# Kernel tuning notes

Hardware: AMD Instinct MI355X
Metric: run time of the kernel (lower is better)

## Reference

```python
import jax, jax.numpy as jnp
import numpy as np

B, N, D, H, DH = 4, 2048, 512, 8, 64  # batch, seqlen, hidden, heads, dim-per-head
EPS = 1e-5


def _layer_norm(x, g, b):
    m = jnp.mean(x, axis=-1, keepdims=True)
    v = jnp.var(x, axis=-1, keepdims=True)
    return (x - m) * jax.lax.rsqrt(v + EPS) * g + b


def setup_inputs() -> dict:
    key = jax.random.key(0)
    k0, k1, k2 = jax.random.split(key, 3)
    T = B * N
    return {
        "x": jax.random.normal(k0, (T, D), jnp.float32),
        "ln1_g": jnp.ones((D,), jnp.float32),
        "ln1_b": jnp.zeros((D,), jnp.float32),
        "w_uvqk": jax.random.normal(k1, (D, H * 4 * DH), jnp.float32) * 0.02,
        "ln2_g": jnp.ones((H * DH,), jnp.float32),
        "ln2_b": jnp.zeros((H * DH,), jnp.float32),
        "w_proj": jax.random.normal(k2, (H * DH, D), jnp.float32) * 0.02,
        "scaling_seqlen": N,
    }


def reference(x, ln1_g, ln1_b, w_uvqk, ln2_g, ln2_b, w_proj, scaling_seqlen):
    T = x.shape[0]
    # input layernorm -> fused uvqk projection -> SiLU
    normed_x = _layer_norm(x, ln1_g, ln1_b)
    silu_uvqk = jax.nn.silu(normed_x @ w_uvqk)          # [T, H*4*DH]
    silu_uvqk = silu_uvqk.reshape(T, H, 4 * DH)
    user, value, query, key = jnp.split(silu_uvqk, [DH, 2 * DH, 3 * DH], axis=-1)

    # jagged -> [B, N, H, DH] (equal-length sequences, offsets = i*N)
    q = query.reshape(B, N, H, DH)
    k = key.reshape(B, N, H, DH)
    v = value.reshape(B, N, H, DH)

    # HSTU attention: silu-gated (no softmax), causal, scaled by 1/scaling_seqlen
    scores = jnp.einsum('bnhd,bmhd->bhnm', q, k)        # [B, H, N, N]
    p = jax.nn.silu(scores) / jnp.float32(scaling_seqlen)
    causal = jnp.tril(jnp.ones((N, N), bool))
    p = jnp.where(causal, p, 0.0)
    attn = jnp.einsum('bhnm,bmhd->bnhd', p, v).reshape(T, H * DH)

    # output norm, user gate, projection, residual (dropout p=0.0 -> identity)
    normed_attn = _layer_norm(attn, ln2_g, ln2_b)
    user_flat = user.reshape(T, H * DH)
    out = (normed_attn * user_flat) @ w_proj + x
    return out
```

## Files before the change

kernel.cpp:

```cpp
#include <hip/hip_runtime.h>
#include <hip/hip_bf16.h>

typedef __bf16 bf16;
typedef __attribute__((ext_vector_type(8))) __bf16 bf16x8;
typedef __attribute__((ext_vector_type(4))) float f32x4;

#define BB   4
#define NN   2048
#define DD   512
#define HH   8
#define DHH  64
#define TT   (BB*NN)
#define NUU  (HH*4*DHH)

#define AS1 __attribute__((address_space(1)))
#define AS3 __attribute__((address_space(3)))
__device__ __forceinline__ void gload16(const void* g, void* l){
  __builtin_amdgcn_global_load_lds((const AS1 void*)g, (AS3 void*)l, 16, 0, 0);
}

__device__ __forceinline__ float silu_fast(float x){
  return x * __builtin_amdgcn_rcpf(1.0f + __expf(-x));
}

__global__ void k_transpose_cast(const float* __restrict__ in, bf16* __restrict__ out,
                                 int R, int C){
  __shared__ float tile[32][33];
  int tx = threadIdx.x, ty = threadIdx.y;
  int c0 = blockIdx.x*32, r0 = blockIdx.y*32;
  #pragma unroll
  for (int i=0;i<4;i++) tile[ty+i*8][tx] = in[(size_t)(r0+ty+i*8)*C + c0+tx];
  __syncthreads();
  #pragma unroll
  for (int i=0;i<4;i++) out[(size_t)(c0+ty+i*8)*R + r0+tx] = (bf16)tile[tx][ty+i*8];
}

__global__ void k_ln_cast(const float* __restrict__ x, const float* __restrict__ g,
                          const float* __restrict__ bta, bf16* __restrict__ out){
  int lane = threadIdx.x & 63;
  int row  = blockIdx.x*4 + (threadIdx.x>>6);
  const float* xr = x + (size_t)row*512 + lane*8;
  float4 v0 = *(const float4*)xr;
  float4 v1 = *(const float4*)(xr+4);
  float vv[8] = {v0.x,v0.y,v0.z,v0.w,v1.x,v1.y,v1.z,v1.w};
  float s = 0.f, ss = 0.f;
  #pragma unroll
  for (int j=0;j<8;j++){ s += vv[j]; ss += vv[j]*vv[j]; }
  #pragma unroll
  for (int d=32; d; d>>=1){ s += __shfl_xor(s,d); ss += __shfl_xor(ss,d); }
  float m  = s * (1.f/512.f);
  float vr = ss * (1.f/512.f) - m*m;
  float rs = rsqrtf(vr + 1e-5f);
  const float* gp = g + lane*8;
  const float* bp = bta + lane*8;
  bf16x8 o;
  #pragma unroll
  for (int j=0;j<8;j++) o[j] = (bf16)((vv[j]-m)*rs*gp[j] + bp[j]);
  *(bf16x8*)(out + (size_t)row*512 + lane*8) = o;
}

__global__ void k_ln_gate(const float* __restrict__ attn, const float* __restrict__ g,
                          const float* __restrict__ bta, const bf16* __restrict__ uvqk,
                          bf16* __restrict__ out){
  int lane = threadIdx.x & 63;
  int row  = blockIdx.x*4 + (threadIdx.x>>6);
  const float* xr = attn + (size_t)row*512 + lane*8;
  float4 v0 = *(const float4*)xr;
  float4 v1 = *(const float4*)(xr+4);
  float vv[8] = {v0.x,v0.y,v0.z,v0.w,v1.x,v1.y,v1.z,v1.w};
  float s = 0.f, ss = 0.f;
  #pragma unroll
  for (int j=0;j<8;j++){ s += vv[j]; ss += vv[j]*vv[j]; }
  #pragma unroll
  for (int d=32; d; d>>=1){ s += __shfl_xor(s,d); ss += __shfl_xor(ss,d); }
  float m  = s * (1.f/512.f);
  float vr = ss * (1.f/512.f) - m*m;
  float rs = rsqrtf(vr + 1e-5f);
  const float* gp = g + lane*8;
  const float* bp = bta + lane*8;
  const bf16* up = uvqk + (size_t)row*NUU + (lane>>3)*256 + ((lane*8)&63);
  bf16x8 uu = *(const bf16x8*)up;
  bf16x8 o;
  #pragma unroll
  for (int j=0;j<8;j++)
    o[j] = (bf16)(((vv[j]-m)*rs*gp[j] + bp[j]) * (float)uu[j]);
  *(bf16x8*)(out + (size_t)row*512 + lane*8) = o;
}

template<int EPI>
__global__ __launch_bounds__(256) void k_gemm(const bf16* __restrict__ A,
                                              const bf16* __restrict__ BT,
                                              int Nd, const float* __restrict__ resid,
                                              void* __restrict__ Cout,
                                              bf16* __restrict__ vtout){
  __shared__ __align__(16) char smem[32768];
  char* As = smem;
  char* Bs = smem + 16384;
  const int K = 512;
  int t = threadIdx.x, lane = t & 63, wid = t >> 6;
  int wr = wid >> 1, wc = wid & 1;
  int lin = blockIdx.x;
  int wk  = (lin & 7)*((int)gridDim.x >> 3) + (lin >> 3);
  int nx  = Nd >> 7;
  int m0 = (wk / nx) * 128, n0 = (wk % nx) * 128;
  int blk = (lane & 7) ^ (lane >> 3);
  const bf16* gA = A  + (size_t)(m0 + wid*32 + (lane>>3))*K + blk*8;
  const bf16* gB = BT + (size_t)(n0 + wid*32 + (lane>>3))*K + blk*8;
  f32x4 acc[4][4] = {};
  for (int k0 = 0; k0 < K; k0 += 64){
    __syncthreads();
    #pragma unroll
    for (int c = 0; c < 4; ++c){
      gload16(gA + (size_t)c*8*K, As + wid*4096 + c*1024);
      gload16(gB + (size_t)c*8*K, Bs + wid*4096 + c*1024);
    }
    gA += 64; gB += 64;
    __syncthreads();
    #pragma unroll
    for (int kk = 0; kk < 64; kk += 32){
      int c0 = kk + (lane >> 4) * 8;
      bf16x8 a[4], b[4];
      #pragma unroll
      for (int i = 0; i < 4; i++){
        int ra = wr*64 + i*16 + (lane & 15);
        a[i] = *(const bf16x8*)(As + (((ra*64 + c0)*2) ^ ((ra & 7) << 4)));
        int rb = wc*64 + i*16 + (lane & 15);
        b[i] = *(const bf16x8*)(Bs + (((rb*64 + c0)*2) ^ ((rb & 7) << 4)));
      }
      #pragma unroll
      for (int i = 0; i < 4; i++)
        #pragma unroll
        for (int jj = 0; jj < 4; jj++)
          acc[i][jj] = __builtin_amdgcn_mfma_f32_16x16x32_bf16(a[i], b[jj], acc[i][jj], 0, 0, 0);
    }
  }
  bool isv = (EPI == 0) && ((n0 & 255) == 0) && (wc == 1);
  #pragma unroll
  for (int i = 0; i < 4; i++){
    #pragma unroll
    for (int jj = 0; jj < 4; jj++){
      int col = n0 + wc*64 + jj*16 + (lane & 15);
      if (EPI == 0){
        union { unsigned long long u; ushort s[4]; } pw;
        #pragma unroll
        for (int r = 0; r < 4; r++){
          int rowg = m0 + wr*64 + i*16 + (lane >> 4)*4 + r;
          float sv = silu_fast(acc[i][jj][r]);
          ((bf16*)Cout)[(size_t)rowg*Nd + col] = (bf16)sv;
          pw.s[r] = __builtin_bit_cast(ushort, (bf16)sv);
        }
        if (isv){
          int dh    = jj*16 + (lane & 15);
          int rowg0 = m0 + wr*64 + i*16 + (lane >> 4)*4;
          int bb = rowg0 >> 11, nn = rowg0 & (NN-1);
          int hh = n0 >> 8;
          *(unsigned long long*)(vtout + ((size_t)((bb*HH + hh)*64 + dh)*NN + nn)) = pw.u;
        }
      } else {
        #pragma unroll
        for (int r = 0; r < 4; r++){
          int rowg = m0 + wr*64 + i*16 + (lane >> 4)*4 + r;
          ((float*)Cout)[(size_t)rowg*Nd + col] = acc[i][jj][r] + resid[(size_t)rowg*Nd + col];
        }
      }
    }
  }
}

__global__ __launch_bounds__(512) void k_attn(const bf16* __restrict__ uv,
                                              const bf16* __restrict__ vt,
                                              float* __restrict__ attn,
                                              const int* __restrict__ scal){
  __shared__ __align__(16) char smem[49152];
  char* Ps = smem + 32768;
  int t = threadIdx.x, lane = t & 63, w = t >> 6;
  int lin  = blockIdx.x;
  int work = (lin & 7)*160 + (lin >> 3);
  int grp  = work / 40;
  int d    = 39 - (work % 40);
  int b = grp >> 3, h = grp & 7;
  int qt, ch;
  if (d < 4)       { qt = d;              ch = 0; }
  else if (d < 12) { qt = 4  + (d-4)/2;   ch = (d-4)&1; }
  else if (d < 24) { qt = 8  + (d-12)/3;  ch = (d-12)%3; }
  else             { qt = 12 + (d-24)/4;  ch = (d-24)&3; }
  int j0 = ch*8;
  int jmax = 2*qt + 1;
  int j1 = (jmax < j0+7) ? jmax : j0+7;
  int tok0 = b*NN + qt*128;
  float sinv = 1.0f / (float)(scal[0]);

  int blk  = (lane & 7) ^ (lane >> 3);
  int rsub = lane >> 3;
  {
    const bf16* gq = uv + (size_t)(tok0 + w*16 + rsub)*NUU + h*256 + 128 + blk*8;
    gload16(gq,         Ps + w*2048);
    gload16(gq + 8*NUU, Ps + w*2048 + 1024);
  }
  const bf16* gk = uv + (size_t)(b*NN + j0*64 + w*8 + rsub)*NUU + h*256 + 192 + blk*8;
  const bf16* gv = vt + (size_t)((b*HH + h)*64 + w*8 + rsub)*NN + j0*64 + blk*8;
  gload16(gk, smem + w*1024);
  gload16(gv, smem + 8192 + w*1024);
  gk += (size_t)64*NUU; gv += 64;
  asm volatile("s_waitcnt vmcnt(0)" ::: "memory");
  __builtin_amdgcn_s_barrier();
  bf16x8 qfrag[2];
  {
    int rq = w*16 + (lane & 15);
    #pragma unroll
    for (int kx = 0; kx < 2; ++kx){
      int c0 = kx*32 + (lane >> 4) * 8;
      qfrag[kx] = *(const bf16x8*)(Ps + (((rq*64 + c0)*2) ^ ((rq & 7) << 4)));
    }
  }
  __syncthreads();

  f32x4 oacc[4] = {};
  int qmin = qt*128 + w*16;
  int q_l  = w*16 + (lane & 15);
  int qglob = qt*128 + q_l;
  int cur = 0;
  for (int j = j0; j <= j1; ++j){
    if (j < j1){
      gload16(gk, smem + (cur^1)*16384 + w*1024);
      gload16(gv, smem + (cur^1)*16384 + 8192 + w*1024);
      gk += (size_t)64*NUU; gv += 64;
      asm volatile("s_waitcnt vmcnt(2)" ::: "memory");
    } else {
      asm volatile("s_waitcnt vmcnt(0)" ::: "memory");
    }
    __builtin_amdgcn_s_barrier();
    char* Ks = smem + cur*16384;
    char* Vs = smem + cur*16384 + 8192;
    if (j*64 < qmin + 16){
      f32x4 sacc[4] = {};
      #pragma unroll
      for (int kx = 0; kx < 2; ++kx){
        int c0 = kx*32 + (lane >> 4) * 8;
        #pragma unroll
        for (int ki = 0; ki < 4; ++ki){
          int rk = ki*16 + (lane & 15);
          bf16x8 ak = *(const bf16x8*)(Ks + (((rk*64 + c0)*2) ^ ((rk & 7) << 4)));
          sacc[ki] = __builtin_amdgcn_mfma_f32_16x16x32_bf16(ak, qfrag[kx], sacc[ki], 0, 0, 0);
        }
      }
      if (j*64 + 63 <= qmin){
        #pragma unroll
        for (int ki = 0; ki < 4; ++ki){
          int kvb = ki*16 + (lane >> 4)*4;
          union { unsigned long long u; ushort s[4]; } pw;
          #pragma unroll
          for (int r = 0; r < 4; r++){
            float p = silu_fast(sacc[ki][r]);
            pw.s[r] = __builtin_bit_cast(ushort, (bf16)p);
          }
          *(unsigned long long*)(Ps + (((q_l*64 + kvb)*2) ^ ((q_l & 7) << 4))) = pw.u;
        }
      } else {
        #pragma unroll
        for (int ki = 0; ki < 4; ++ki){
          int kvb = ki*16 + (lane >> 4)*4;
          union { unsigned long long u; ushort s[4]; } pw;
          #pragma unroll
          for (int r = 0; r < 4; r++){
            float p = ((j*64 + kvb + r) <= qglob) ? silu_fast(sacc[ki][r]) : 0.0f;
            pw.s[r] = __builtin_bit_cast(ushort, (bf16)p);
          }
          *(unsigned long long*)(Ps + (((q_l*64 + kvb)*2) ^ ((q_l & 7) << 4))) = pw.u;
        }
      }
      #pragma unroll
      for (int kk = 0; kk < 64; kk += 32){
        int c0 = kk + (lane >> 4) * 8;
        bf16x8 pa = *(const bf16x8*)(Ps + (((q_l*64 + c0)*2) ^ ((q_l & 7) << 4)));
        #pragma unroll
        for (int ni = 0; ni < 4; ++ni){
          int rv = ni*16 + (lane & 15);
          bf16x8 vb = *(const bf16x8*)(Vs + (((rv*64 + c0)*2) ^ ((rv & 7) << 4)));
          oacc[ni] = __builtin_amdgcn_mfma_f32_16x16x32_bf16(pa, vb, oacc[ni], 0, 0, 0);
        }
      }
    }
    asm volatile("" ::: "memory");
    __builtin_amdgcn_s_barrier();
    cur ^= 1;
  }
  #pragma unroll
  for (int ni = 0; ni < 4; ++ni)
    #pragma unroll
    for (int r = 0; r < 4; r++)
      atomicAdd(&attn[(size_t)(tok0 + w*16 + (lane >> 4)*4 + r)*DD + h*64 + ni*16 + (lane & 15)],
                oacc[ni][r] * sinv);
}

extern "C" void kernel_launch(void* const* d_in, const int* in_sizes, int n_in,
                              void* d_out, int out_size, void* d_ws, size_t ws_size,
                              hipStream_t stream){
  (void)in_sizes; (void)n_in; (void)out_size; (void)ws_size;
  const float* x      = (const float*)d_in[0];
  const float* ln1_g  = (const float*)d_in[1];
  const float* ln1_b  = (const float*)d_in[2];
  const float* w_uvqk = (const float*)d_in[3];
  const float* ln2_g  = (const float*)d_in[4];
  const float* ln2_b  = (const float*)d_in[5];
  const float* w_proj = (const float*)d_in[6];
  const int*   scal   = (const int*)d_in[7];
  float* out = (float*)d_out;

  char* ws = (char*)d_ws;
  bf16*  wT1  = (bf16*)(ws);
  bf16*  wT2  = (bf16*)(ws + (2u<<20));
  bf16*  xn   = (bf16*)(ws + (2u<<20) + (512u<<10));
  bf16*  uvq  = (bf16*)(ws + (10u<<20) + (512u<<10));
  float* attn = (float*)(ws + (42u<<20) + (512u<<10));
  bf16*  vtb  = (bf16*)(ws + (58u<<20) + (512u<<10));

  hipMemsetAsync(attn, 0, (size_t)TT*DD*sizeof(float), stream);
  k_transpose_cast<<<dim3(64,16), dim3(32,8), 0, stream>>>(w_uvqk, wT1, 512, 2048);
  k_transpose_cast<<<dim3(16,16), dim3(32,8), 0, stream>>>(w_proj, wT2, 512, 512);
  k_ln_cast<<<TT/4, 256, 0, stream>>>(x, ln1_g, ln1_b, xn);
  k_gemm<0><<<dim3(1024), dim3(256), 0, stream>>>(xn, wT1, 2048, nullptr, (void*)uvq, vtb);
  k_attn<<<dim3(1280), dim3(512), 0, stream>>>(uvq, vtb, attn, scal);
  k_ln_gate<<<TT/4, 256, 0, stream>>>(attn, ln2_g, ln2_b, uvq, xn);
  k_gemm<1><<<dim3(256), dim3(256), 0, stream>>>(xn, wT2, 512, x, (void*)out, nullptr);
}
```

Before: 113.6 us.

## Rewrite HSTU attention with 32x32 MFMA and register-resident P via permlane swap

The attention kernel moves from 16x16x32 to 32x32x16 bf16 MFMA tiles, with each of 4 waves (256 threads) owning 32 query rows instead of 8 waves owning 16. The silu-gated score tile is packed to bf16 in registers and redistributed with v_permlane32_swap, so it feeds the PV MFMA directly instead of round-tripping through an LDS P buffer. This cuts LDS traffic and shared memory to 32KB and sets launch bounds for 4 blocks per CU. In exchange it raises register pressure from larger accumulators, and each wave now issues twice as many K/V loads per tile.

```diff
diff --git a/kernel.cpp b/kernel.cpp
--- a/kernel.cpp
+++ b/kernel.cpp
@@ -4,6 +4,7 @@
 typedef __bf16 bf16;
 typedef __attribute__((ext_vector_type(8))) __bf16 bf16x8;
 typedef __attribute__((ext_vector_type(4))) float f32x4;
+typedef __attribute__((ext_vector_type(16))) float f32x16;
 
 #define BB   4
 #define NN   2048
@@ -21,6 +22,15 @@
 
 __device__ __forceinline__ float silu_fast(float x){
   return x * __builtin_amdgcn_rcpf(1.0f + __expf(-x));
+}
+
+__device__ __forceinline__ unsigned pk2(float a, float b){
+  return (unsigned)__builtin_bit_cast(unsigned short, (bf16)a)
+       | ((unsigned)__builtin_bit_cast(unsigned short, (bf16)b) << 16);
+}
+
+__device__ __forceinline__ void plswap(unsigned &a, unsigned &b){
+  asm volatile("v_permlane32_swap_b32 %0, %1" : "+v"(a), "+v"(b));
 }
 
 __global__ void k_transpose_cast(const float* __restrict__ in, bf16* __restrict__ out,
@@ -167,13 +177,13 @@
   }
 }
 
-__global__ __launch_bounds__(512) void k_attn(const bf16* __restrict__ uv,
-                                              const bf16* __restrict__ vt,
-                                              float* __restrict__ attn,
-                                              const int* __restrict__ scal){
-  __shared__ __align__(16) char smem[49152];
-  char* Ps = smem + 32768;
+__global__ __launch_bounds__(256, 4) void k_attn(const bf16* __restrict__ uv,
+                                                 const bf16* __restrict__ vt,
+                                                 float* __restrict__ attn,
+                                                 const int* __restrict__ scal){
+  __shared__ __align__(16) char smem[32768];
   int t = threadIdx.x, lane = t & 63, w = t >> 6;
+  int hi5 = lane >> 5;
   int lin  = blockIdx.x;
   int work = (lin & 7)*160 + (lin >> 3);
   int grp  = work / 40;
@@ -192,92 +202,94 @@
 
   int blk  = (lane & 7) ^ (lane >> 3);
   int rsub = lane >> 3;
+
   {
-    const bf16* gq = uv + (size_t)(tok0 + w*16 + rsub)*NUU + h*256 + 128 + blk*8;
-    gload16(gq,         Ps + w*2048);
-    gload16(gq + 8*NUU, Ps + w*2048 + 1024);
-  }
-  const bf16* gk = uv + (size_t)(b*NN + j0*64 + w*8 + rsub)*NUU + h*256 + 192 + blk*8;
-  const bf16* gv = vt + (size_t)((b*HH + h)*64 + w*8 + rsub)*NN + j0*64 + blk*8;
-  gload16(gk, smem + w*1024);
-  gload16(gv, smem + 8192 + w*1024);
+    const bf16* gq = uv + (size_t)(tok0 + w*32 + rsub)*NUU + h*256 + 128 + blk*8;
+    #pragma unroll
+    for (int i = 0; i < 4; ++i)
+      gload16(gq + (size_t)i*8*NUU, smem + 16384 + w*4096 + i*1024);
+  }
+  const bf16* gk = uv + (size_t)(b*NN + j0*64 + w*16 + rsub)*NUU + h*256 + 192 + blk*8;
+  const bf16* gv = vt + (size_t)((b*HH + h)*64 + w*16 + rsub)*NN + j0*64 + blk*8;
+  gload16(gk,                  smem + w*2048);
+  gload16(gk + (size_t)8*NUU,  smem + w*2048 + 1024);
+  gload16(gv,                  smem + 8192 + w*2048);
+  gload16(gv + (size_t)8*NN,   smem + 8192 + w*2048 + 1024);
   gk += (size_t)64*NUU; gv += 64;
-  asm volatile("s_waitcnt vmcnt(0)" ::: "memory");
-  __builtin_amdgcn_s_barrier();
-  bf16x8 qfrag[2];
+  asm volatile("s_waitcnt vmcnt(4)" ::: "memory");
+  bf16x8 qfrag[4];
   {
-    int rq = w*16 + (lane & 15);
-    #pragma unroll
-    for (int kx = 0; kx < 2; ++kx){
-      int c0 = kx*32 + (lane >> 4) * 8;
-      qfrag[kx] = *(const bf16x8*)(Ps + (((rq*64 + c0)*2) ^ ((rq & 7) << 4)));
+    int rq = w*32 + (lane & 31);
+    char* Qs = smem + 16384;
+    #pragma unroll
+    for (int ks = 0; ks < 4; ++ks){
+      int c0 = ks*16 + hi5*8;
+      qfrag[ks] = *(const bf16x8*)(Qs + (((rq*64 + c0)*2) ^ ((rq & 7) << 4)));
     }
   }
   __syncthreads();
 
-  f32x4 oacc[4] = {};
-  int qmin = qt*128 + w*16;
-  int q_l  = w*16 + (lane & 15);
-  int qglob = qt*128 + q_l;
+  f32x16 oacc[2] = {};
+  int qmin  = qt*128 + w*32;
+  int qglob = qmin + (lane & 31);
   int cur = 0;
   for (int j = j0; j <= j1; ++j){
     if (j < j1){
-      gload16(gk, smem + (cur^1)*16384 + w*1024);
-      gload16(gv, smem + (cur^1)*16384 + 8192 + w*1024);
+      gload16(gk,                 smem + (cur^1)*16384 + w*2048);
+      gload16(gk + (size_t)8*NUU, smem + (cur^1)*16384 + w*2048 + 1024);
+      gload16(gv,                 smem + (cur^1)*16384 + 8192 + w*2048);
+      gload16(gv + (size_t)8*NN,  smem + (cur^1)*16384 + 8192 + w*2048 + 1024);
       gk += (size_t)64*NUU; gv += 64;
-      asm volatile("s_waitcnt vmcnt(2)" ::: "memory");
+      asm volatile("s_waitcnt vmcnt(4)" ::: "memory");
     } else {
       asm volatile("s_waitcnt vmcnt(0)" ::: "memory");
     }
     __builtin_amdgcn_s_barrier();
     char* Ks = smem + cur*16384;
-    char* Vs = smem + cur*16384 + 8192;
-    if (j*64 < qmin + 16){
-      f32x4 sacc[4] = {};
-      #pragma unroll
-      for (int kx = 0; kx < 2; ++kx){
-        int c0 = kx*32 + (lane >> 4) * 8;
-        #pragma unroll
-        for (int ki = 0; ki < 4; ++ki){
-          int rk = ki*16 + (lane & 15);
+    char* Vs = Ks + 8192;
+    #pragma unroll
+    for (int sub = 0; sub < 2; ++sub){
+      int kvbase = j*64 + sub*32;
+      if (kvbase < qmin + 32){
+        f32x16 sacc = {};
+        int rk = sub*32 + (lane & 31);
+        #pragma unroll
+        for (int ks = 0; ks < 4; ++ks){
+          int c0 = ks*16 + hi5*8;
           bf16x8 ak = *(const bf16x8*)(Ks + (((rk*64 + c0)*2) ^ ((rk & 7) << 4)));
-          sacc[ki] = __builtin_amdgcn_mfma_f32_16x16x32_bf16(ak, qfrag[kx], sacc[ki], 0, 0, 0);
-        }
-      }
-      if (j*64 + 63 <= qmin){
-        #pragma unroll
-        for (int ki = 0; ki < 4; ++ki){
-          int kvb = ki*16 + (lane >> 4)*4;
-          union { unsigned long long u; ushort s[4]; } pw;
+          sacc = __builtin_amdgcn_mfma_f32_32x32x16_bf16(ak, qfrag[ks], sacc, 0, 0, 0);
+        }
+        union { unsigned u[8]; bf16x8 v[2]; } P;
+        if (kvbase + 31 <= qmin){
           #pragma unroll
-          for (int r = 0; r < 4; r++){
-            float p = silu_fast(sacc[ki][r]);
-            pw.s[r] = __builtin_bit_cast(ushort, (bf16)p);
+          for (int m = 0; m < 4; ++m){
+            P.u[2*m]   = pk2(silu_fast(sacc[4*m+0]), silu_fast(sacc[4*m+1]));
+            P.u[2*m+1] = pk2(silu_fast(sacc[4*m+2]), silu_fast(sacc[4*m+3]));
           }
-          *(unsigned long long*)(Ps + (((q_l*64 + kvb)*2) ^ ((q_l & 7) << 4))) = pw.u;
-        }
-      } else {
-        #pragma unroll
-        for (int ki = 0; ki < 4; ++ki){
-          int kvb = ki*16 + (lane >> 4)*4;
-          union { unsigned long long u; ushort s[4]; } pw;
+        } else {
           #pragma unroll
-          for (int r = 0; r < 4; r++){
-            float p = ((j*64 + kvb + r) <= qglob) ? silu_fast(sacc[ki][r]) : 0.0f;
-            pw.s[r] = __builtin_bit_cast(ushort, (bf16)p);
+          for (int m = 0; m < 4; ++m){
+            float pr[4];
+            #pragma unroll
+            for (int r = 0; r < 4; ++r){
+              int kvg = kvbase + 8*m + 4*hi5 + r;
+              pr[r] = (kvg <= qglob) ? silu_fast(sacc[4*m+r]) : 0.0f;
+            }
+            P.u[2*m]   = pk2(pr[0], pr[1]);
+            P.u[2*m+1] = pk2(pr[2], pr[3]);
           }
-          *(unsigned long long*)(Ps + (((q_l*64 + kvb)*2) ^ ((q_l & 7) << 4))) = pw.u;
-        }
-      }
-      #pragma unroll
-      for (int kk = 0; kk < 64; kk += 32){
-        int c0 = kk + (lane >> 4) * 8;
-        bf16x8 pa = *(const bf16x8*)(Ps + (((q_l*64 + c0)*2) ^ ((q_l & 7) << 4)));
-        #pragma unroll
-        for (int ni = 0; ni < 4; ++ni){
-          int rv = ni*16 + (lane & 15);
-          bf16x8 vb = *(const bf16x8*)(Vs + (((rv*64 + c0)*2) ^ ((rv & 7) << 4)));
-          oacc[ni] = __builtin_amdgcn_mfma_f32_16x16x32_bf16(pa, vb, oacc[ni], 0, 0, 0);
+        }
+        plswap(P.u[0], P.u[2]); plswap(P.u[1], P.u[3]);
+        plswap(P.u[4], P.u[6]); plswap(P.u[5], P.u[7]);
+        #pragma unroll
+        for (int kh = 0; kh < 2; ++kh){
+          int c0 = sub*32 + kh*16 + hi5*8;
+          #pragma unroll
+          for (int dsb = 0; dsb < 2; ++dsb){
+            int rv = dsb*32 + (lane & 31);
+            bf16x8 vb = *(const bf16x8*)(Vs + (((rv*64 + c0)*2) ^ ((rv & 7) << 4)));
+            oacc[dsb] = __builtin_amdgcn_mfma_f32_32x32x16_bf16(P.v[kh], vb, oacc[dsb], 0, 0, 0);
+          }
         }
       }
     }
@@ -286,11 +298,14 @@
     cur ^= 1;
   }
   #pragma unroll
-  for (int ni = 0; ni < 4; ++ni)
-    #pragma unroll
-    for (int r = 0; r < 4; r++)
-      atomicAdd(&attn[(size_t)(tok0 + w*16 + (lane >> 4)*4 + r)*DD + h*64 + ni*16 + (lane & 15)],
-                oacc[ni][r] * sinv);
+  for (int dsb = 0; dsb < 2; ++dsb){
+    #pragma unroll
+    for (int r = 0; r < 16; ++r){
+      int qrow = (r & 3) + 4*hi5 + 8*(r >> 2);
+      atomicAdd(&attn[(size_t)(tok0 + w*32 + qrow)*DD + h*64 + dsb*32 + (lane & 31)],
+                oacc[dsb][r] * sinv);
+    }
+  }
 }
 
 extern "C" void kernel_launch(void* const* d_in, const int* in_sizes, int n_in,
@@ -320,7 +335,7 @@
   k_transpose_cast<<<dim3(16,16), dim3(32,8), 0, stream>>>(w_proj, wT2, 512, 512);
   k_ln_cast<<<TT/4, 256, 0, stream>>>(x, ln1_g, ln1_b, xn);
   k_gemm<0><<<dim3(1024), dim3(256), 0, stream>>>(xn, wT1, 2048, nullptr, (void*)uvq, vtb);
-  k_attn<<<dim3(1280), dim3(512), 0, stream>>>(uvq, vtb, attn, scal);
+  k_attn<<<dim3(1280), dim3(256), 0, stream>>>(uvq, vtb, attn, scal);
   k_ln_gate<<<TT/4, 256, 0, stream>>>(attn, ln2_g, ln2_b, uvq, xn);
   k_gemm<1><<<dim3(256), dim3(256), 0, stream>>>(xn, wT2, 512, x, (void*)out, nullptr);
 }
```

After: 113.2 us. No clear change (-0.3%).
